# Performance work log

Hardware: AMD Instinct MI355X
Metric: run time of the kernel (lower is better)

The kernel has to match this reference:

```python
import jax, jax.numpy as jnp
import numpy as np

N, P, E, D, T, R, K = 4096, 32768, 4096, 128, 3, 4, 16
CURRENT_TIME = 1.0


def setup_inputs() -> dict:
    key = jax.random.key(0)
    ks = jax.random.split(key, 12)
    pairs = jax.random.randint(ks[0], (P, 2), 0, N)
    adj = (jax.random.randint(ks[1], (N, N), 0, 100) == 0).astype(jnp.int32)
    adj = jnp.maximum(adj, adj.T) * (1 - jnp.eye(N, dtype=jnp.int32))
    neigh_idx = jax.random.randint(ks[2], (N, R, K), 0, N)
    node_type = jax.random.randint(ks[3], (N,), 0, T)
    # event timestamps far in the past so the decay sum stays O(1)
    t_events = -(jax.random.uniform(ks[4], (E,), dtype=jnp.float32) * 100.0 + 50.0)
    node_embeds = 0.1 * jax.random.normal(ks[5], (N, D), dtype=jnp.float32)
    W_proj = 0.1 * jax.random.normal(ks[6], (T, D, D), dtype=jnp.float32)
    W_beta = 0.1 * jax.random.normal(ks[7], (R, D, D), dtype=jnp.float32)
    b_beta = 0.1 * jax.random.normal(ks[8], (R, D), dtype=jnp.float32)
    decay_theta = jnp.float32(0.1)
    q1 = jnp.float32(0.5)
    q2 = jnp.float32(0.1)
    return dict(pairs=pairs, adj=adj, neigh_idx=neigh_idx, node_type=node_type,
                t_events=t_events, node_embeds=node_embeds, W_proj=W_proj,
                W_beta=W_beta, b_beta=b_beta, decay_theta=decay_theta, q1=q1, q2=q2)


def _forward(pairs, adj, neigh_idx, node_type, t_events, node_embeds,
             W_proj, W_beta, b_beta, decay_theta, q1, q2):
    n_nodes, d = node_embeds.shape
    adj_f = adj.astype(node_embeds.dtype)
    pm, pn = pairs[:, 0], pairs[:, 1]

    # --- HistoricalEdgeModule: type-specific projection + global decay sum ---
    proj_all = jnp.einsum('nd,tde->tne', node_embeds, W_proj)      # [T,N,D]
    proj = proj_all[node_type, jnp.arange(n_nodes)]                # [N,D]
    diff = proj[pm] - proj[pn]
    gamma_base = -jnp.sqrt(jnp.sum(diff * diff, axis=-1))          # [P]
    sum_alpha = jnp.sum(jnp.exp(-decay_theta * (CURRENT_TIME - t_events)))
    lambda_hist = gamma_base + sum_alpha                           # [P]

    # --- TriadicClosureModule: clustering coeff + common-neighbor sum ---
    deg = adj_f.sum(axis=1)
    tri = jnp.sum((adj_f @ adj_f) * adj_f.T, axis=1)               # diag(A^3)
    denom = deg * (deg - 1.0)
    denom = jnp.where(denom == 0, 1e-6, denom)
    C = 2.0 * tri / denom                                          # [N]
    common = adj_f[pm] * adj_f[pn]                                 # [P,N] common-neighbor mask
    Csum = common @ C                                              # [P]
    g = -jnp.sum((node_embeds[pm] - node_embeds[pn]) ** 2, axis=-1)
    lambda_tri = Csum * g                                          # [P]

    # --- NeighborInfluenceModule: per-relation mean agg -> macro sigmoid ---
    h_r = node_embeds[neigh_idx].mean(axis=2)                      # [N,R,D]
    h_agg = jnp.einsum('nrd,rde->nre', h_r, W_beta) + b_beta       # [N,R,D]
    eps = jax.nn.sigmoid(h_agg.mean(axis=1))                       # [N,D]
    lambda_neigh = jnp.sum(eps[pm] * eps[pn], axis=-1) / d         # [P]

    lam = jnp.exp(lambda_hist + lambda_tri + lambda_neigh)
    return jax.nn.sigmoid(q1 * lam + q2)


def reference(pairs, adj, neigh_idx, node_type, t_events, node_embeds,
              W_proj, W_beta, b_beta, decay_theta, q1, q2):
    return _forward(pairs, adj, neigh_idx, node_type, t_events, node_embeds,
                    W_proj, W_beta, b_beta, decay_theta, q1, q2)
```

## Files before the change

kernel.cpp:

```cpp
#include <hip/hip_runtime.h>
#include <math.h>

#define N_NODES 4096
#define DIM     128
#define NPAIRS  32768
#define NEVENTS 4096
#define NTYPES  3
#define NREL    4
#define NNEIGH  16
#define WORDS   64
#define MAXDEG  192


#define PA_MASK_END  (N_NODES / 4)
#define PA_PROJ_END  (PA_MASK_END + N_NODES / 2)
#define PA_HR_END    (PA_PROJ_END + N_NODES * NREL * DIM / 256)
#define PA_TOTAL     (PA_HR_END + 1)

__global__ __launch_bounds__(256) void k_phaseA(const int* __restrict__ adj,
                                                unsigned long long* __restrict__ mask,
                                                float* __restrict__ degf,
                                                unsigned short* __restrict__ nbr,
                                                const float* __restrict__ x,
                                                const int* __restrict__ ntype,
                                                const float* __restrict__ Wp,
                                                float* __restrict__ proj,
                                                const int* __restrict__ nidx,
                                                float* __restrict__ h,
                                                const float* __restrict__ t_events,
                                                const float* __restrict__ theta_p,
                                                float* __restrict__ salpha) {
    __shared__ float smem[512];
    int b = blockIdx.x;

    if (b < PA_MASK_END) {
        int wave = threadIdx.x >> 6;
        int lane = threadIdx.x & 63;
        int row  = b * 4 + wave;
        const int4* arow = (const int4*)(adj + (size_t)row * N_NODES);
        unsigned long long myw = 0ULL;
        #pragma unroll
        for (int ch = 0; ch < 16; ++ch) {
            int4 v = arow[ch * 64 + lane];
            unsigned long long b0 = __ballot(v.x != 0);
            unsigned long long b1 = __ballot(v.y != 0);
            unsigned long long b2 = __ballot(v.z != 0);
            unsigned long long b3 = __ballot(v.w != 0);
            if ((lane >> 2) == ch) {
                int c = lane & 3;
                myw = (c == 0) ? b0 : (c == 1) ? b1 : (c == 2) ? b2 : b3;
            }
        }
        mask[(size_t)row * WORDS + lane] = myw;
        int pc = (int)__popcll(myw);
        int scan = pc;
        #pragma unroll
        for (int off = 1; off < 64; off <<= 1) {
            int nv = __shfl_up(scan, off);
            if (lane >= off) scan += nv;
        }
        int excl = scan - pc;
        if (lane == 63) degf[row] = (float)scan;
        unsigned short* nl = nbr + (size_t)row * MAXDEG;
        int jb = (lane >> 2) * 256 + (lane & 3);
        unsigned long long ww = myw;
        int o = excl;
        while (ww) {
            int bit = __ffsll(ww) - 1;
            nl[o++] = (unsigned short)(jb + bit * 4);
            ww &= ww - 1;
        }

    } else if (b < PA_PROJ_END) {
        int base = (b - PA_MASK_END) * 2;
        int g = threadIdx.x >> 7;
        int e = threadIdx.x & 127;
        int n = base + g;
        float* xs = smem;
        xs[g * DIM + e] = x[(size_t)n * DIM + e];
        __syncthreads();
        int t = ntype[n];
        const float* W = Wp + (size_t)t * DIM * DIM + e;
        float acc = 0.f;
        #pragma unroll 8
        for (int d = 0; d < DIM; ++d)
            acc += xs[g * DIM + d] * W[(size_t)d * DIM];
        proj[(size_t)n * DIM + e] = acc;

    } else if (b < PA_HR_END) {
        int tid = (b - PA_PROJ_END) * 256 + threadIdx.x;
        int d  = tid & (DIM - 1);
        int nr = tid >> 7;
        const int4* idx4 = (const int4*)(nidx + (size_t)nr * NNEIGH);
        int4 i0 = idx4[0], i1 = idx4[1], i2 = idx4[2], i3 = idx4[3];
        float s = 0.f;
        s += x[(size_t)i0.x * DIM + d]; s += x[(size_t)i0.y * DIM + d];
        s += x[(size_t)i0.z * DIM + d]; s += x[(size_t)i0.w * DIM + d];
        s += x[(size_t)i1.x * DIM + d]; s += x[(size_t)i1.y * DIM + d];
        s += x[(size_t)i1.z * DIM + d]; s += x[(size_t)i1.w * DIM + d];
        s += x[(size_t)i2.x * DIM + d]; s += x[(size_t)i2.y * DIM + d];
        s += x[(size_t)i2.z * DIM + d]; s += x[(size_t)i2.w * DIM + d];
        s += x[(size_t)i3.x * DIM + d]; s += x[(size_t)i3.y * DIM + d];
        s += x[(size_t)i3.z * DIM + d]; s += x[(size_t)i3.w * DIM + d];
        h[tid] = s * (1.0f / 16.0f);

    } else {
        float th = theta_p[0];
        float acc = 0.f;
        for (int i = threadIdx.x; i < NEVENTS; i += 256)
            acc += expf(-th * (1.0f - t_events[i]));
        smem[threadIdx.x] = acc;
        __syncthreads();
        for (int s = 128; s > 0; s >>= 1) {
            if (threadIdx.x < s) smem[threadIdx.x] += smem[threadIdx.x + s];
            __syncthreads();
        }
        if (threadIdx.x == 0) salpha[0] = smem[0];
    }
}

__global__ __launch_bounds__(256) void k_phaseB(const unsigned long long* __restrict__ mask,
                                                const float* __restrict__ degf,
                                                const unsigned short* __restrict__ nbr,
                                                float* __restrict__ C,
                                                const float* __restrict__ h,
                                                const float* __restrict__ Wb,
                                                const float* __restrict__ bb,
                                                float* __restrict__ eps) {
    __shared__ float smem[6144];
    int b = blockIdx.x;

    if (b < N_NODES / 4) {
        int wave = threadIdx.x >> 6;
        int lane = threadIdx.x & 63;
        int node = b * 4 + wave;
        unsigned long long my = mask[(size_t)node * WORDS + lane];
        int dg = (int)degf[node];
        const unsigned short* nl = nbr + (size_t)node * MAXDEG;
        int i0 = nl[lane], i1 = nl[64 + lane], i2 = nl[128 + lane];
        unsigned int acc = 0;
        #pragma unroll 4
        for (int it = 0; it < dg; ++it) {
            int sel = (it < 64) ? i0 : (it < 128) ? i1 : i2;
            int j = __shfl(sel, it & 63);
            acc += __popcll(my & mask[(size_t)j * WORDS + lane]);
        }
        for (int off = 32; off > 0; off >>= 1) acc += __shfl_xor(acc, off);
        if (lane == 0) {
            float dgF = (float)dg;
            float denom = dgF * (dgF - 1.0f);
            if (denom == 0.0f) denom = 1e-6f;
            C[node] = 2.0f * (float)acc / denom;
        }

    } else {
        int base = (b - N_NODES / 4) * 8;
        int e = threadIdx.x & 127;
        int g = threadIdx.x >> 7;
        float* hs = smem;
        float* part = smem + 4096;
        const float4* hsrc = (const float4*)(h + (size_t)base * NREL * DIM);
        float4* hs4 = (float4*)hs;
        #pragma unroll
        for (int i = 0; i < 4; ++i) hs4[threadIdx.x + i * 256] = hsrc[threadIdx.x + i * 256];
        __syncthreads();
        const float* W = Wb + (size_t)(g * 256) * DIM + e;
        const float4* h4 = (const float4*)hs;
        int kq = g * 64;
        float a[8] = {0.f, 0.f, 0.f, 0.f, 0.f, 0.f, 0.f, 0.f};
        #pragma unroll 2
        for (int kg = 0; kg < 64; ++kg) {
            float w0 = W[(size_t)(4 * kg + 0) * DIM];
            float w1 = W[(size_t)(4 * kg + 1) * DIM];
            float w2 = W[(size_t)(4 * kg + 2) * DIM];
            float w3 = W[(size_t)(4 * kg + 3) * DIM];
            #pragma unroll
            for (int m = 0; m < 8; ++m) {
                float4 hv = h4[m * 128 + kq + kg];
                a[m] += hv.x * w0 + hv.y * w1 + hv.z * w2 + hv.w * w3;
            }
        }
        #pragma unroll
        for (int m = 0; m < 8; ++m) part[(g * 8 + m) * 128 + e] = a[m];
        __syncthreads();
        if (g == 0) {
            float bsum = bb[e] + bb[DIM + e] + bb[2 * DIM + e] + bb[3 * DIM + e];
            #pragma unroll
            for (int m = 0; m < 8; ++m) {
                float v = (part[m * 128 + e] + part[(8 + m) * 128 + e] + bsum) * 0.25f;
                eps[(size_t)(base + m) * DIM + e] = 1.0f / (1.0f + expf(-v));
            }
        }
    }
}

__global__ __launch_bounds__(256) void k_pairs(const int* __restrict__ pairs,
                                               const unsigned long long* __restrict__ mask,
                                               const float* __restrict__ C,
                                               const float* __restrict__ proj,
                                               const float* __restrict__ eps,
                                               const float* __restrict__ x,
                                               const float* __restrict__ salpha_p,
                                               const float* __restrict__ q1p,
                                               const float* __restrict__ q2p,
                                               float* __restrict__ out) {
    int wave = threadIdx.x >> 6;
    int lane = threadIdx.x & 63;
    int p = blockIdx.x * 4 + wave;
    int pm = pairs[p * 2];
    int pn = pairs[p * 2 + 1];

    unsigned long long cw = mask[(size_t)pm * WORDS + lane] & mask[(size_t)pn * WORDS + lane];
    float csum = 0.f;
    int jbase = (lane >> 2) * 256 + (lane & 3);
    while (cw) {
        int bit = __ffsll(cw) - 1;
        csum += C[jbase + bit * 4];
        cw &= cw - 1;
    }

    const float2* Am = (const float2*)(proj + (size_t)pm * DIM);
    const float2* An = (const float2*)(proj + (size_t)pn * DIM);
    const float2* Xm = (const float2*)(x    + (size_t)pm * DIM);
    const float2* Xn = (const float2*)(x    + (size_t)pn * DIM);
    const float2* Em = (const float2*)(eps  + (size_t)pm * DIM);
    const float2* En = (const float2*)(eps  + (size_t)pn * DIM);
    float2 am = Am[lane], an = An[lane];
    float2 xm = Xm[lane], xn = Xn[lane];
    float2 em = Em[lane], en = En[lane];

    float dpx = am.x - an.x, dpy = am.y - an.y;
    float s1 = dpx * dpx + dpy * dpy;
    float dxx = xm.x - xn.x, dxy = xm.y - xn.y;
    float s2 = dxx * dxx + dxy * dxy;
    float s3 = em.x * en.x + em.y * en.y;

    for (int off = 32; off > 0; off >>= 1) {
        s1 += __shfl_xor(s1, off);
        s2 += __shfl_xor(s2, off);
        s3 += __shfl_xor(s3, off);
        csum += __shfl_xor(csum, off);
    }
    if (lane == 0) {
        float lhist  = -sqrtf(s1) + salpha_p[0];
        float ltri   = csum * (-s2);
        float lneigh = s3 * (1.0f / 128.0f);
        float lam = expf(lhist + ltri + lneigh);
        float z = q1p[0] * lam + q2p[0];
        out[p] = 1.0f / (1.0f + expf(-z));
    }
}

extern "C" void kernel_launch(void* const* d_in, const int* in_sizes, int n_in,
                              void* d_out, int out_size, void* d_ws, size_t ws_size,
                              hipStream_t stream) {
    const int*   pairs    = (const int*)d_in[0];
    const int*   adj      = (const int*)d_in[1];
    const int*   nidx     = (const int*)d_in[2];
    const int*   ntype    = (const int*)d_in[3];
    const float* t_events = (const float*)d_in[4];
    const float* x        = (const float*)d_in[5];
    const float* Wp       = (const float*)d_in[6];
    const float* Wb       = (const float*)d_in[7];
    const float* bb       = (const float*)d_in[8];
    const float* theta    = (const float*)d_in[9];
    const float* q1       = (const float*)d_in[10];
    const float* q2       = (const float*)d_in[11];
    float* out = (float*)d_out;

    char* ws = (char*)d_ws;
    unsigned long long* mask = (unsigned long long*)(ws + 0);
    float* deg    = (float*)(ws + 2097152);
    float* C      = (float*)(ws + 2113536);
    float* proj   = (float*)(ws + 2129920);
    float* eps    = (float*)(ws + 4227072);
    float* salpha = (float*)(ws + 6324224);
    float* h      = (float*)(ws + 6324352);
    unsigned short* nbr = (unsigned short*)(ws + 14712960);

    hipLaunchKernelGGL(k_phaseA, dim3(PA_TOTAL),              dim3(256), 0, stream,
                       adj, mask, deg, nbr, x, ntype, Wp, proj, nidx, h, t_events, theta, salpha);
    hipLaunchKernelGGL(k_phaseB, dim3(N_NODES / 4 + N_NODES / 8), dim3(256), 0, stream,
                       mask, deg, nbr, C, h, Wb, bb, eps);
    hipLaunchKernelGGL(k_pairs,  dim3(NPAIRS / 4),            dim3(256), 0, stream,
                       pairs, mask, C, proj, eps, x, salpha, q1, q2, out);
}
```

Baseline: 95.14 us.

## Split triangle count across four waves per node and halve eps rows per block

The clustering-coefficient part of phase B now gives each node a whole 256-thread block instead of one wave. The four waves take interleaved neighbors and are combined through shared memory. The eps GEMV path processes 4 nodes per block instead of 8, with half the shared memory, which raises the block count and occupancy. The cost is more blocks, an extra block-level sync per node, and more reloads of W_beta per node in the eps path.

```diff
diff --git a/kernel.cpp b/kernel.cpp
--- a/kernel.cpp
+++ b/kernel.cpp
@@ -127,67 +127,77 @@
                                                 const float* __restrict__ Wb,
                                                 const float* __restrict__ bb,
                                                 float* __restrict__ eps) {
-    __shared__ float smem[6144];
+    __shared__ float smem[3072];
     int b = blockIdx.x;
 
-    if (b < N_NODES / 4) {
+    if (b < N_NODES) {
         int wave = threadIdx.x >> 6;
         int lane = threadIdx.x & 63;
-        int node = b * 4 + wave;
+        int node = b;
         unsigned long long my = mask[(size_t)node * WORDS + lane];
         int dg = (int)degf[node];
         const unsigned short* nl = nbr + (size_t)node * MAXDEG;
-        int i0 = nl[lane], i1 = nl[64 + lane], i2 = nl[128 + lane];
+        int pidx = wave + 4 * lane;
+        int pre = (lane < 48) ? (int)nl[pidx] : 0;
+        int nit = (dg - wave + 3) >> 2;
+        if (nit < 0) nit = 0;
         unsigned int acc = 0;
         #pragma unroll 4
-        for (int it = 0; it < dg; ++it) {
-            int sel = (it < 64) ? i0 : (it < 128) ? i1 : i2;
-            int j = __shfl(sel, it & 63);
+        for (int t = 0; t < nit; ++t) {
+            int j = __shfl(pre, t);
             acc += __popcll(my & mask[(size_t)j * WORDS + lane]);
         }
         for (int off = 32; off > 0; off >>= 1) acc += __shfl_xor(acc, off);
-        if (lane == 0) {
+        unsigned int* wacc = (unsigned int*)smem;
+        if (lane == 0) wacc[wave] = acc;
+        __syncthreads();
+        if (threadIdx.x == 0) {
+            float tri = (float)(wacc[0] + wacc[1] + wacc[2] + wacc[3]);
             float dgF = (float)dg;
             float denom = dgF * (dgF - 1.0f);
             if (denom == 0.0f) denom = 1e-6f;
-            C[node] = 2.0f * (float)acc / denom;
+            C[node] = 2.0f * tri / denom;
         }
 
     } else {
-        int base = (b - N_NODES / 4) * 8;
+        int base = (b - N_NODES) * 4;
         int e = threadIdx.x & 127;
         int g = threadIdx.x >> 7;
         float* hs = smem;
-        float* part = smem + 4096;
+        float* part = smem + 2048;
         const float4* hsrc = (const float4*)(h + (size_t)base * NREL * DIM);
         float4* hs4 = (float4*)hs;
-        #pragma unroll
-        for (int i = 0; i < 4; ++i) hs4[threadIdx.x + i * 256] = hsrc[threadIdx.x + i * 256];
+        for (int i = threadIdx.x; i < 512; i += 256) hs4[i] = hsrc[i];
         __syncthreads();
         const float* W = Wb + (size_t)(g * 256) * DIM + e;
         const float4* h4 = (const float4*)hs;
         int kq = g * 64;
-        float a[8] = {0.f, 0.f, 0.f, 0.f, 0.f, 0.f, 0.f, 0.f};
-        #pragma unroll 2
+        float a0 = 0.f, a1 = 0.f, a2 = 0.f, a3 = 0.f;
+        #pragma unroll 4
         for (int kg = 0; kg < 64; ++kg) {
             float w0 = W[(size_t)(4 * kg + 0) * DIM];
             float w1 = W[(size_t)(4 * kg + 1) * DIM];
             float w2 = W[(size_t)(4 * kg + 2) * DIM];
             float w3 = W[(size_t)(4 * kg + 3) * DIM];
-            #pragma unroll
-            for (int m = 0; m < 8; ++m) {
-                float4 hv = h4[m * 128 + kq + kg];
-                a[m] += hv.x * w0 + hv.y * w1 + hv.z * w2 + hv.w * w3;
-            }
-        }
-        #pragma unroll
-        for (int m = 0; m < 8; ++m) part[(g * 8 + m) * 128 + e] = a[m];
+            float4 h0 = h4[0 * 128 + kq + kg];
+            float4 h1 = h4[1 * 128 + kq + kg];
+            float4 h2 = h4[2 * 128 + kq + kg];
+            float4 h3 = h4[3 * 128 + kq + kg];
+            a0 += h0.x * w0 + h0.y * w1 + h0.z * w2 + h0.w * w3;
+            a1 += h1.x * w0 + h1.y * w1 + h1.z * w2 + h1.w * w3;
+            a2 += h2.x * w0 + h2.y * w1 + h2.z * w2 + h2.w * w3;
+            a3 += h3.x * w0 + h3.y * w1 + h3.z * w2 + h3.w * w3;
+        }
+        part[(g * 4 + 0) * 128 + e] = a0;
+        part[(g * 4 + 1) * 128 + e] = a1;
+        part[(g * 4 + 2) * 128 + e] = a2;
+        part[(g * 4 + 3) * 128 + e] = a3;
         __syncthreads();
         if (g == 0) {
             float bsum = bb[e] + bb[DIM + e] + bb[2 * DIM + e] + bb[3 * DIM + e];
             #pragma unroll
-            for (int m = 0; m < 8; ++m) {
-                float v = (part[m * 128 + e] + part[(8 + m) * 128 + e] + bsum) * 0.25f;
+            for (int m = 0; m < 4; ++m) {
+                float v = (part[m * 128 + e] + part[(4 + m) * 128 + e] + bsum) * 0.25f;
                 eps[(size_t)(base + m) * DIM + e] = 1.0f / (1.0f + expf(-v));
             }
         }
@@ -280,7 +290,7 @@
 
     hipLaunchKernelGGL(k_phaseA, dim3(PA_TOTAL),              dim3(256), 0, stream,
                        adj, mask, deg, nbr, x, ntype, Wp, proj, nidx, h, t_events, theta, salpha);
-    hipLaunchKernelGGL(k_phaseB, dim3(N_NODES / 4 + N_NODES / 8), dim3(256), 0, stream,
+    hipLaunchKernelGGL(k_phaseB, dim3(N_NODES + N_NODES / 4), dim3(256), 0, stream,
                        mask, deg, nbr, C, h, Wb, bb, eps);
     hipLaunchKernelGGL(k_pairs,  dim3(NPAIRS / 4),            dim3(256), 0, stream,
                        pairs, mask, C, proj, eps, x, salpha, q1, q2, out);
```

Measured after the change: 87.50 us. 1.09x faster.
